# Performance work log

Hardware: AMD Instinct MI355X
Metric: run time of the kernel (lower is better)

The kernel has to match this reference:

```python
import jax, jax.numpy as jnp
import numpy as np

EMBED_DIM = 1024
HEAD_SIZE = 128


def setup_inputs() -> dict:
    key = jax.random.key(0)
    k1, k2, k3, k4 = jax.random.split(key, 4)
    B, T, C = 8, 2048, EMBED_DIM
    x = jax.random.normal(k1, (B, T, C), dtype=jnp.float32)
    # torch Linear(in, out, bias=False): weight shape [out, in]
    s = 1.0 / np.sqrt(C)
    Wk = jax.random.uniform(k2, (HEAD_SIZE, C), jnp.float32, -s, s)
    Wq = jax.random.uniform(k3, (HEAD_SIZE, C), jnp.float32, -s, s)
    Wv = jax.random.uniform(k4, (HEAD_SIZE, C), jnp.float32, -s, s)
    return {"x": x, "Wk": Wk, "Wq": Wq, "Wv": Wv}


def reference(x, Wk, Wq, Wv):
    B, T, C = x.shape
    k = jnp.einsum('btc,hc->bth', x, Wk)  # [B,T,H]
    q = jnp.einsum('btc,hc->bth', x, Wq)
    v = jnp.einsum('btc,hc->bth', x, Wv)
    # NOTE: original scales by C**-0.5 with C = embedding dim (not head size)
    w = jnp.einsum('bth,bsh->bts', q, k) * (C ** -0.5)  # [B,T,T]
    causal = jnp.tril(jnp.ones((T, T), dtype=bool))
    w = jnp.where(causal, w, -jnp.inf)
    w = jax.nn.softmax(w, axis=-1)
    return jnp.einsum('bts,bsh->bth', w, v)
```

## Files before the change

### kernel.cpp

```cpp
#include <hip/hip_runtime.h>
#include <stdint.h>

#define BATCH 8
#define SEQ   2048
#define EMB   1024
#define HD    128

typedef __attribute__((ext_vector_type(8))) short  s8v;
typedef __attribute__((ext_vector_type(4))) float  f4v;

__device__ __forceinline__ ushort cvt_bf16(float f) {
    union { float f; uint32_t u; } v; v.f = f;
    uint32_t r = v.u + 0x7FFFu + ((v.u >> 16) & 1u);
    return (ushort)(r >> 16);
}

__device__ __forceinline__ uint32_t pack_bf16(float lo, float hi) {
    return ((uint32_t)cvt_bf16(hi) << 16) | (uint32_t)cvt_bf16(lo);
}

__device__ __forceinline__ f4v mfma16(s8v a, s8v b, f4v c) {
    return __builtin_amdgcn_mfma_f32_16x16x32_bf16(a, b, c, 0, 0, 0);
}

__device__ __forceinline__ uint32_t bperm(int idx, uint32_t v) {
    return (uint32_t)__builtin_amdgcn_ds_bpermute(idx, (int)v);
}

__device__ __forceinline__ void gl_lds16(const void* g, void* l) {
    __builtin_amdgcn_global_load_lds(
        (const __attribute__((address_space(1))) void*)g,
        (__attribute__((address_space(3))) void*)l, 16, 0, 0);
}

__global__ __launch_bounds__(256) void wcvt_kernel(
    const float* __restrict__ Wk, const float* __restrict__ Wq,
    const float* __restrict__ Wv, ushort* __restrict__ Wb)
{
    const int row = blockIdx.x;
    const float* __restrict__ src =
        (row < 128) ? Wk + (size_t)row * EMB :
        (row < 256) ? Wq + (size_t)(row - 128) * EMB :
                      Wv + (size_t)(row - 256) * EMB;
    const int c = threadIdx.x << 2;
    float4 f = *(const float4*)(src + c);
    ushort4 h;
    h.x = cvt_bf16(f.x); h.y = cvt_bf16(f.y);
    h.z = cvt_bf16(f.z); h.w = cvt_bf16(f.w);
    *(ushort4*)(Wb + (size_t)row * EMB + c) = h;
}

__global__ __launch_bounds__(256) void qkv_kernel(
    const float* __restrict__ x,
    const ushort* __restrict__ Wb,
    ushort* __restrict__ Kg,
    ushort* __restrict__ Qg,
    ushort* __restrict__ VTg)
{
    const int m0 = blockIdx.x * 32;
    __shared__ ushort Al[32][68];
    __shared__ ushort Bl[384 * 64];

    const int tid  = threadIdx.x;
    const int lane = tid & 63;
    const int wave = tid >> 6;
    const int lr = lane & 15, lg = lane >> 4;
    const int xsw = (lr & 7) << 4;

    f4v acc[2][6] = {};

    const char* gW[12];
    #pragma unroll
    for (int c = 0; c < 12; ++c) {
        int cc   = wave * 12 + c;
        int row  = cc * 8 + (lane >> 3);
        int colb = ((lane & 7) << 4) ^ ((row & 7) << 4);
        gW[c] = (const char*)Wb + (size_t)row * (EMB * 2) + colb;
    }
    const int ar = tid >> 3, ac = (tid & 7) << 3;
    const float* xp = x + (size_t)(m0 + ar) * EMB + ac;

    for (int k0 = 0; k0 < EMB; k0 += 64) {
        #pragma unroll
        for (int c = 0; c < 12; ++c) {
            gl_lds16(gW[c], (char*)Bl + ((wave * 12 + c) << 10));
            gW[c] += 128;
        }
        float4 f0 = *(const float4*)(xp);
        float4 f1 = *(const float4*)(xp + 4);
        xp += 64;
        ushort4 h0, h1;
        h0.x = cvt_bf16(f0.x); h0.y = cvt_bf16(f0.y);
        h0.z = cvt_bf16(f0.z); h0.w = cvt_bf16(f0.w);
        h1.x = cvt_bf16(f1.x); h1.y = cvt_bf16(f1.y);
        h1.z = cvt_bf16(f1.z); h1.w = cvt_bf16(f1.w);
        *(ushort4*)&Al[ar][ac]     = h0;
        *(ushort4*)&Al[ar][ac + 4] = h1;
        __syncthreads();

        #pragma unroll
        for (int kk = 0; kk < 2; ++kk) {
            s8v af[2], bf[6];
            #pragma unroll
            for (int i = 0; i < 2; ++i)
                af[i] = *(const s8v*)&Al[16 * i + lr][32 * kk + 8 * lg];
            #pragma unroll
            for (int j = 0; j < 6; ++j) {
                int row = 96 * wave + 16 * j + lr;
                bf[j] = *(const s8v*)((const char*)Bl + (row << 7)
                                      + ((kk * 64 + lg * 16) ^ xsw));
            }
            #pragma unroll
            for (int i = 0; i < 2; ++i)
                #pragma unroll
                for (int j = 0; j < 6; ++j)
                    acc[i][j] = mfma16(af[i], bf[j], acc[i][j]);
        }
        __syncthreads();
    }

    const int b  = m0 >> 11;
    const int tb = m0 & 2047;
    #pragma unroll
    for (int j = 0; j < 6; ++j) {
        const int n   = 96 * wave + 16 * j + lr;
        const int sel = n >> 7;
        const int h   = n & 127;
        if (sel < 2) {
            ushort* __restrict__ outp = sel ? Qg : Kg;
            #pragma unroll
            for (int i = 0; i < 2; ++i)
                #pragma unroll
                for (int reg = 0; reg < 4; ++reg) {
                    int m = m0 + 16 * i + 4 * lg + reg;
                    outp[(size_t)m * HD + h] = cvt_bf16(acc[i][j][reg]);
                }
        } else {
            #pragma unroll
            for (int i = 0; i < 2; ++i) {
                int t = tb + 16 * i + 4 * lg;
                ushort4 hv;
                hv.x = cvt_bf16(acc[i][j][0]);
                hv.y = cvt_bf16(acc[i][j][1]);
                hv.z = cvt_bf16(acc[i][j][2]);
                hv.w = cvt_bf16(acc[i][j][3]);
                *(ushort4*)(VTg + ((size_t)b * HD + h) * SEQ + t) = hv;
            }
        }
    }
}

__global__ __launch_bounds__(256) void attn_kernel(
    const ushort* __restrict__ Qg,
    const ushort* __restrict__ Kg,
    const ushort* __restrict__ VTg,
    ushort* __restrict__ o_part,
    float2* __restrict__ ml_part,
    int cts, int NCH)
{
    int s = blockIdx.x, g = 0;
    while (s >= ((g + 1) << cts)) { s -= (g + 1) << cts; ++g; }
    int q2 = 0;
    while (s >= g + 1) { s -= g + 1; ++q2; }
    const int jq = (g << cts) + q2;
    const int ch = s;
    const int b  = blockIdx.y;
    const int t0 = ch << cts;
    const int t1 = min(t0 + (1 << cts), jq + 1);

    const int tid  = threadIdx.x;
    const int lane = tid & 63;
    const int wave = tid >> 6;
    const int lr = lane & 15, lg = lane >> 4;
    const int xsw = (lr & 7) << 4;

    __shared__ ushort kl[2][64 * 128];
    __shared__ ushort vl[2][128 * 64];

    const ushort* __restrict__ Qb = Qg  + (size_t)b * SEQ * HD;
    const ushort* __restrict__ Kb = Kg  + (size_t)b * SEQ * HD;
    const ushort* __restrict__ Vb = VTg + (size_t)b * HD * SEQ;

    const char* gK[4];
    const char* gV[4];
    #pragma unroll
    for (int c = 0; c < 4; ++c) {
        int cc = wave * 4 + c;
        {   int row  = cc * 4 + (lane >> 4);
            int colb = ((lane & 15) << 4) ^ ((row & 7) << 4);
            gK[c] = (const char*)Kb + (size_t)(t0 * 64 + row) * 256 + colb; }
        {   int row  = cc * 8 + (lane >> 3);
            int colb = ((lane & 7) << 4) ^ ((row & 7) << 4);
            gV[c] = (const char*)Vb + (size_t)row * (SEQ * 2)
                    + (size_t)t0 * 128 + colb; }
    }

    const int qw    = jq * 64 + wave * 16;
    const int q_abs = qw + lr;

    s8v qf[4];
    #pragma unroll
    for (int f = 0; f < 4; ++f)
        qf[f] = *(const s8v*)(Qb + (size_t)(qw + lr) * HD + 32 * f + 8 * lg);

    f4v o[8] = {};
    float m_r = -1e30f, l_r = 0.0f;

    #pragma unroll
    for (int c = 0; c < 4; ++c) {
        gl_lds16(gK[c], (char*)(&kl[0][0]) + ((wave * 4 + c) << 10));
        gl_lds16(gV[c], (char*)(&vl[0][0]) + ((wave * 4 + c) << 10));
        gK[c] += 64 * 256;
        gV[c] += 128;
    }
    __syncthreads();

    const int i0 = ((2 * (lg & 1)) * 16 + lr) << 2;
    const int i1 = ((2 * (lg & 1) + 1) * 16 + lr) << 2;
    const bool hi = (lg >= 2);

    int cur = 0;
    for (int st = t0; st < t1; ++st) {
        if (st + 1 < t1) {
            char* kb = (char*)(&kl[cur ^ 1][0]);
            char* vb = (char*)(&vl[cur ^ 1][0]);
            #pragma unroll
            for (int c = 0; c < 4; ++c) {
                gl_lds16(gK[c], kb + ((wave * 4 + c) << 10));
                gl_lds16(gV[c], vb + ((wave * 4 + c) << 10));
                gK[c] += 64 * 256;
                gV[c] += 128;
            }
        }
        const int s0 = st * 64;
        const char* klb = (const char*)(&kl[cur][0]);
        const char* vlb = (const char*)(&vl[cur][0]);

        f4v sc[4] = {};
        #pragma unroll
        for (int sf = 0; sf < 4; ++sf)
            #pragma unroll
            for (int kf = 0; kf < 4; ++kf) {
                s8v kfr = *(const s8v*)(klb + ((sf * 16 + lr) << 8)
                                        + ((kf * 64 + lg * 16) ^ xsw));
                sc[sf] = mfma16(kfr, qf[kf], sc[sf]);
            }

        float p[4][4];
        const bool diag = (st == jq);
        #pragma unroll
        for (int sf = 0; sf < 4; ++sf)
            #pragma unroll
            for (int reg = 0; reg < 4; ++reg) {
                float v = sc[sf][reg] * 0.03125f;
                if (diag && (s0 + sf * 16 + 4 * lg + reg) > q_abs) v = -1e30f;
                p[sf][reg] = v;
            }

        float pm = p[0][0];
        #pragma unroll
        for (int sf = 0; sf < 4; ++sf)
            #pragma unroll
            for (int reg = 0; reg < 4; ++reg) pm = fmaxf(pm, p[sf][reg]);
        pm = fmaxf(pm, __shfl_xor(pm, 16));
        pm = fmaxf(pm, __shfl_xor(pm, 32));
        const float mnew = fmaxf(m_r, pm);
        const float fac  = __expf(m_r - mnew);
        m_r = mnew;

        float ls = 0.0f;
        #pragma unroll
        for (int sf = 0; sf < 4; ++sf)
            #pragma unroll
            for (int reg = 0; reg < 4; ++reg) {
                p[sf][reg] = __expf(p[sf][reg] - mnew);
                ls += p[sf][reg];
            }
        ls += __shfl_xor(ls, 16);
        ls += __shfl_xor(ls, 32);
        l_r = l_r * fac + ls;
        #pragma unroll
        for (int hf = 0; hf < 8; ++hf) o[hf] *= fac;

        uint32_t pk[4][2];
        #pragma unroll
        for (int sf = 0; sf < 4; ++sf) {
            pk[sf][0] = pack_bf16(p[sf][0], p[sf][1]);
            pk[sf][1] = pack_bf16(p[sf][2], p[sf][3]);
        }

        #pragma unroll
        for (int s2 = 0; s2 < 2; ++s2) {
            uint32_t a0 = bperm(i0, pk[2 * s2][0]);
            uint32_t a1 = bperm(i0, pk[2 * s2][1]);
            uint32_t a2 = bperm(i1, pk[2 * s2][0]);
            uint32_t a3 = bperm(i1, pk[2 * s2][1]);
            uint32_t b0 = bperm(i0, pk[2 * s2 + 1][0]);
            uint32_t b1 = bperm(i0, pk[2 * s2 + 1][1]);
            uint32_t b2 = bperm(i1, pk[2 * s2 + 1][0]);
            uint32_t b3 = bperm(i1, pk[2 * s2 + 1][1]);
            union { int4 i; s8v h; } pb;
            pb.i.x = (int)(hi ? b0 : a0);
            pb.i.y = (int)(hi ? b1 : a1);
            pb.i.z = (int)(hi ? b2 : a2);
            pb.i.w = (int)(hi ? b3 : a3);
            #pragma unroll
            for (int hf = 0; hf < 8; ++hf) {
                s8v vf = *(const s8v*)(vlb + ((hf * 16 + lr) << 7)
                                       + ((s2 * 64 + lg * 16) ^ xsw));
                o[hf] = mfma16(vf, pb.h, o[hf]);
            }
        }

        __syncthreads();
        cur ^= 1;
    }

    const size_t pbase = ((size_t)(b * 32 + jq) * NCH + ch) * 64;
    const int q = wave * 16 + lr;
    if (lg == 0) {
        float2 v; v.x = m_r; v.y = l_r;
        ml_part[pbase + q] = v;
    }
    #pragma unroll
    for (int hf = 0; hf < 8; ++hf) {
        ushort4 hv;
        hv.x = cvt_bf16(o[hf][0]);
        hv.y = cvt_bf16(o[hf][1]);
        hv.z = cvt_bf16(o[hf][2]);
        hv.w = cvt_bf16(o[hf][3]);
        *(ushort4*)(o_part + (pbase + q) * HD + hf * 16 + 4 * lg) = hv;
    }
}

__global__ __launch_bounds__(256) void combine_kernel(
    const ushort* __restrict__ o_part,
    const float2* __restrict__ ml_part,
    float* __restrict__ out, int cts, int NCH)
{
    const int tid = threadIdx.x;
    const int R   = blockIdx.x * 16 + (tid >> 4);
    const int c16 = tid & 15;
    const int b  = R >> 11;
    const int rq = R & 2047;
    const int jq = rq >> 6;
    const int r  = rq & 63;
    const int nch = (jq >> cts) + 1;

    const size_t mlbase = ((size_t)(b * 32 + jq) * NCH) * 64 + r;

    float M = -1e30f;
    for (int c = 0; c < nch; ++c)
        M = fmaxf(M, ml_part[mlbase + (size_t)c * 64].x);
    float L = 0.0f;
    for (int c = 0; c < nch; ++c) {
        float2 v = ml_part[mlbase + (size_t)c * 64];
        L += v.y * __expf(v.x - M);
    }
    const float invL = 1.0f / L;

    float acc[8];
    #pragma unroll
    for (int k = 0; k < 8; ++k) acc[k] = 0.0f;

    for (int c = 0; c < nch; ++c) {
        float2 v = ml_part[mlbase + (size_t)c * 64];
        float sc = __expf(v.x - M) * invL;
        s8v pv = *(const s8v*)(o_part + (mlbase + (size_t)c * 64) * HD + c16 * 8);
        #pragma unroll
        for (int j = 0; j < 8; ++j) {
            union { uint32_t u; float f; } cv;
            cv.u = ((uint32_t)(ushort)pv[j]) << 16;
            acc[j] += cv.f * sc;
        }
    }

    float* po = out + (size_t)R * HD + c16 * 8;
    *(float4*)(po)     = make_float4(acc[0], acc[1], acc[2], acc[3]);
    *(float4*)(po + 4) = make_float4(acc[4], acc[5], acc[6], acc[7]);
}

extern "C" void kernel_launch(void* const* d_in, const int* in_sizes, int n_in,
                              void* d_out, int out_size, void* d_ws, size_t ws_size,
                              hipStream_t stream) {
    const float* x  = (const float*)d_in[0];
    const float* Wk = (const float*)d_in[1];
    const float* Wq = (const float*)d_in[2];
    const float* Wv = (const float*)d_in[3];

    const size_t qkv_elems = (size_t)BATCH * SEQ * HD;
    const size_t wb_elems  = (size_t)384 * EMB;
    ushort* Kg  = (ushort*)d_ws;
    ushort* Qg  = Kg + qkv_elems;
    ushort* VTg = Qg + qkv_elems;
    float*  outp = (float*)d_out;

    int cts = 2, NCH = 8;
    {
        size_t rows = (size_t)BATCH * 32 * NCH * 64;
        size_t need = 3 * qkv_elems * sizeof(ushort)
                    + rows * (HD * sizeof(ushort) + sizeof(float2))
                    + wb_elems * sizeof(ushort);
        if (ws_size < need) { cts = 3; NCH = 4; }
    }
    size_t part_rows = (size_t)BATCH * 32 * NCH * 64;
    ushort* o_part  = VTg + qkv_elems;
    float2* ml_part = (float2*)(o_part + part_rows * HD);
    ushort* Wb      = (ushort*)(ml_part + part_rows);

    const int G = 32 >> cts;
    const int slots = (1 << cts) * G * (G + 1) / 2;

    wcvt_kernel<<<384, 256, 0, stream>>>(Wk, Wq, Wv, Wb);
    qkv_kernel<<<512, 256, 0, stream>>>(x, Wb, Kg, Qg, VTg);
    dim3 g2(slots, BATCH);
    attn_kernel<<<g2, 256, 0, stream>>>(Qg, Kg, VTg, o_part, ml_part, cts, NCH);
    combine_kernel<<<1024, 256, 0, stream>>>(o_part, ml_part, outp, cts, NCH);
}
```

Baseline: 81.97 us.

## Load QKV GEMM operands directly from global into registers, dropping LDS staging

The QKV projection kernel no longer stages x and the bf16 weights through shared memory with barriers. Each lane now loads its MFMA fragments straight from global memory, converting x with packed bf16 intrinsics, and relies on the cache for reuse across waves. This removes the LDS traffic and the __syncthreads stalls. The cost is uncoalesced, strided global loads, with every wave re-reading the same x rows from cache.

```diff
diff --git a/kernel.cpp b/kernel.cpp
--- a/kernel.cpp
+++ b/kernel.cpp
@@ -1,4 +1,5 @@
 #include <hip/hip_runtime.h>
+#include <hip/hip_bf16.h>
 #include <stdint.h>
 
 #define BATCH 8
@@ -31,6 +32,15 @@
     __builtin_amdgcn_global_load_lds(
         (const __attribute__((address_space(1))) void*)g,
         (__attribute__((address_space(3))) void*)l, 16, 0, 0);
+}
+
+__device__ __forceinline__ s8v cvt8(float4 a, float4 b) {
+    union { s8v h; __hip_bfloat162 p[4]; } u;
+    u.p[0] = __float22bfloat162_rn(make_float2(a.x, a.y));
+    u.p[1] = __float22bfloat162_rn(make_float2(a.z, a.w));
+    u.p[2] = __float22bfloat162_rn(make_float2(b.x, b.y));
+    u.p[3] = __float22bfloat162_rn(make_float2(b.z, b.w));
+    return u.h;
 }
 
 __global__ __launch_bounds__(256) void wcvt_kernel(
@@ -58,65 +68,35 @@
     ushort* __restrict__ VTg)
 {
     const int m0 = blockIdx.x * 32;
-    __shared__ ushort Al[32][68];
-    __shared__ ushort Bl[384 * 64];
-
     const int tid  = threadIdx.x;
     const int lane = tid & 63;
     const int wave = tid >> 6;
     const int lr = lane & 15, lg = lane >> 4;
-    const int xsw = (lr & 7) << 4;
 
     f4v acc[2][6] = {};
 
-    const char* gW[12];
-    #pragma unroll
-    for (int c = 0; c < 12; ++c) {
-        int cc   = wave * 12 + c;
-        int row  = cc * 8 + (lane >> 3);
-        int colb = ((lane & 7) << 4) ^ ((row & 7) << 4);
-        gW[c] = (const char*)Wb + (size_t)row * (EMB * 2) + colb;
-    }
-    const int ar = tid >> 3, ac = (tid & 7) << 3;
-    const float* xp = x + (size_t)(m0 + ar) * EMB + ac;
-
-    for (int k0 = 0; k0 < EMB; k0 += 64) {
-        #pragma unroll
-        for (int c = 0; c < 12; ++c) {
-            gl_lds16(gW[c], (char*)Bl + ((wave * 12 + c) << 10));
-            gW[c] += 128;
-        }
-        float4 f0 = *(const float4*)(xp);
-        float4 f1 = *(const float4*)(xp + 4);
-        xp += 64;
-        ushort4 h0, h1;
-        h0.x = cvt_bf16(f0.x); h0.y = cvt_bf16(f0.y);
-        h0.z = cvt_bf16(f0.z); h0.w = cvt_bf16(f0.w);
-        h1.x = cvt_bf16(f1.x); h1.y = cvt_bf16(f1.y);
-        h1.z = cvt_bf16(f1.z); h1.w = cvt_bf16(f1.w);
-        *(ushort4*)&Al[ar][ac]     = h0;
-        *(ushort4*)&Al[ar][ac + 4] = h1;
-        __syncthreads();
-
-        #pragma unroll
-        for (int kk = 0; kk < 2; ++kk) {
-            s8v af[2], bf[6];
-            #pragma unroll
-            for (int i = 0; i < 2; ++i)
-                af[i] = *(const s8v*)&Al[16 * i + lr][32 * kk + 8 * lg];
-            #pragma unroll
-            for (int j = 0; j < 6; ++j) {
-                int row = 96 * wave + 16 * j + lr;
-                bf[j] = *(const s8v*)((const char*)Bl + (row << 7)
-                                      + ((kk * 64 + lg * 16) ^ xsw));
-            }
-            #pragma unroll
-            for (int i = 0; i < 2; ++i)
-                #pragma unroll
-                for (int j = 0; j < 6; ++j)
-                    acc[i][j] = mfma16(af[i], bf[j], acc[i][j]);
-        }
-        __syncthreads();
+    const float* xp0 = x + (size_t)(m0 + lr) * EMB + 8 * lg;
+    const float* xp1 = xp0 + (size_t)16 * EMB;
+    const ushort* wp0 = Wb + (size_t)(96 * wave + lr) * EMB + 8 * lg;
+
+    #pragma unroll 4
+    for (int ks = 0; ks < 32; ++ks) {
+        const int kc = ks * 32;
+        float4 a0 = *(const float4*)(xp0 + kc);
+        float4 a1 = *(const float4*)(xp0 + kc + 4);
+        float4 b0 = *(const float4*)(xp1 + kc);
+        float4 b1 = *(const float4*)(xp1 + kc + 4);
+        s8v af0 = cvt8(a0, a1);
+        s8v af1 = cvt8(b0, b1);
+        s8v bf[6];
+        #pragma unroll
+        for (int j = 0; j < 6; ++j)
+            bf[j] = *(const s8v*)(wp0 + (size_t)j * 16 * EMB + kc);
+        #pragma unroll
+        for (int j = 0; j < 6; ++j) {
+            acc[0][j] = mfma16(af0, bf[j], acc[0][j]);
+            acc[1][j] = mfma16(af1, bf[j], acc[1][j]);
+        }
     }
 
     const int b  = m0 >> 11;
```

New measurement: 127.3 us. 55.3% more time.

## Retile QKV projection into 128x128 per-weight output tiles

Applied to the files above, without the earlier changes.

The QKV GEMM now gives each block a 128-row by 128-column tile of a single projection (K, Q or V), with a 4x4 MFMA tile per wave, instead of 32 rows across all 384 output columns. This raises MFMA work per loaded element and cuts the total weight re-reads. In exchange x is read three times, and the async global-to-LDS weight loads and XOR swizzle are replaced by plain synchronous loads into padded shared memory. The grid shrinks to 384 blocks.

```diff
diff --git a/kernel.cpp b/kernel.cpp
--- a/kernel.cpp
+++ b/kernel.cpp
@@ -1,4 +1,5 @@
 #include <hip/hip_runtime.h>
+#include <hip/hip_bf16.h>
 #include <stdint.h>
 
 #define BATCH 8
@@ -57,96 +58,91 @@
     ushort* __restrict__ Qg,
     ushort* __restrict__ VTg)
 {
-    const int m0 = blockIdx.x * 32;
-    __shared__ ushort Al[32][68];
-    __shared__ ushort Bl[384 * 64];
+    const int bid  = blockIdx.x;
+    const int rest = bid >> 3;
+    const int wsel = rest % 3;
+    const int mt   = ((rest / 3) << 3) | (bid & 7);
+    const int m0 = mt * 128;
+    const ushort* __restrict__ Wp = Wb + (size_t)wsel * 128 * EMB;
+
+    __shared__ ushort Al[128][72];
+    __shared__ ushort Bl[128][72];
 
     const int tid  = threadIdx.x;
     const int lane = tid & 63;
     const int wave = tid >> 6;
+    const int wm = wave >> 1, wn = wave & 1;
     const int lr = lane & 15, lg = lane >> 4;
-    const int xsw = (lr & 7) << 4;
-
-    f4v acc[2][6] = {};
-
-    const char* gW[12];
-    #pragma unroll
-    for (int c = 0; c < 12; ++c) {
-        int cc   = wave * 12 + c;
-        int row  = cc * 8 + (lane >> 3);
-        int colb = ((lane & 7) << 4) ^ ((row & 7) << 4);
-        gW[c] = (const char*)Wb + (size_t)row * (EMB * 2) + colb;
-    }
-    const int ar = tid >> 3, ac = (tid & 7) << 3;
-    const float* xp = x + (size_t)(m0 + ar) * EMB + ac;
+
+    f4v acc[4][4] = {};
 
     for (int k0 = 0; k0 < EMB; k0 += 64) {
         #pragma unroll
-        for (int c = 0; c < 12; ++c) {
-            gl_lds16(gW[c], (char*)Bl + ((wave * 12 + c) << 10));
-            gW[c] += 128;
-        }
-        float4 f0 = *(const float4*)(xp);
-        float4 f1 = *(const float4*)(xp + 4);
-        xp += 64;
-        ushort4 h0, h1;
-        h0.x = cvt_bf16(f0.x); h0.y = cvt_bf16(f0.y);
-        h0.z = cvt_bf16(f0.z); h0.w = cvt_bf16(f0.w);
-        h1.x = cvt_bf16(f1.x); h1.y = cvt_bf16(f1.y);
-        h1.z = cvt_bf16(f1.z); h1.w = cvt_bf16(f1.w);
-        *(ushort4*)&Al[ar][ac]     = h0;
-        *(ushort4*)&Al[ar][ac + 4] = h1;
+        for (int it = 0; it < 8; ++it) {
+            int chunk = tid + 256 * it;
+            int r  = chunk >> 4;
+            int c4 = (chunk & 15) << 2;
+            float4 fa = *(const float4*)(x + (size_t)(m0 + r) * EMB + k0 + c4);
+            ushort4 ha;
+            ha.x = cvt_bf16(fa.x); ha.y = cvt_bf16(fa.y);
+            ha.z = cvt_bf16(fa.z); ha.w = cvt_bf16(fa.w);
+            *(ushort4*)&Al[r][c4] = ha;
+        }
+        #pragma unroll
+        for (int it = 0; it < 4; ++it) {
+            int chunk = tid + 256 * it;
+            int r  = chunk >> 3;
+            int c8 = (chunk & 7) << 3;
+            *(int4*)&Bl[r][c8] = *(const int4*)(Wp + (size_t)r * EMB + k0 + c8);
+        }
         __syncthreads();
-
         #pragma unroll
         for (int kk = 0; kk < 2; ++kk) {
-            s8v af[2], bf[6];
-            #pragma unroll
-            for (int i = 0; i < 2; ++i)
-                af[i] = *(const s8v*)&Al[16 * i + lr][32 * kk + 8 * lg];
-            #pragma unroll
-            for (int j = 0; j < 6; ++j) {
-                int row = 96 * wave + 16 * j + lr;
-                bf[j] = *(const s8v*)((const char*)Bl + (row << 7)
-                                      + ((kk * 64 + lg * 16) ^ xsw));
-            }
-            #pragma unroll
-            for (int i = 0; i < 2; ++i)
+            s8v af[4], bf[4];
+            #pragma unroll
+            for (int i = 0; i < 4; ++i)
+                af[i] = *(const s8v*)&Al[64 * wm + 16 * i + lr][32 * kk + 8 * lg];
+            #pragma unroll
+            for (int j = 0; j < 4; ++j)
+                bf[j] = *(const s8v*)&Bl[64 * wn + 16 * j + lr][32 * kk + 8 * lg];
+            #pragma unroll
+            for (int i = 0; i < 4; ++i)
                 #pragma unroll
-                for (int j = 0; j < 6; ++j)
+                for (int j = 0; j < 4; ++j)
                     acc[i][j] = mfma16(af[i], bf[j], acc[i][j]);
         }
         __syncthreads();
     }
 
-    const int b  = m0 >> 11;
-    const int tb = m0 & 2047;
-    #pragma unroll
-    for (int j = 0; j < 6; ++j) {
-        const int n   = 96 * wave + 16 * j + lr;
-        const int sel = n >> 7;
-        const int h   = n & 127;
-        if (sel < 2) {
-            ushort* __restrict__ outp = sel ? Qg : Kg;
-            #pragma unroll
-            for (int i = 0; i < 2; ++i)
+    if (wsel < 2) {
+        ushort* __restrict__ outp = wsel ? Qg : Kg;
+        #pragma unroll
+        for (int i = 0; i < 4; ++i)
+            #pragma unroll
+            for (int j = 0; j < 4; ++j) {
+                int h = 64 * wn + 16 * j + lr;
                 #pragma unroll
                 for (int reg = 0; reg < 4; ++reg) {
-                    int m = m0 + 16 * i + 4 * lg + reg;
+                    int m = m0 + 64 * wm + 16 * i + 4 * lg + reg;
                     outp[(size_t)m * HD + h] = cvt_bf16(acc[i][j][reg]);
                 }
-        } else {
-            #pragma unroll
-            for (int i = 0; i < 2; ++i) {
-                int t = tb + 16 * i + 4 * lg;
+            }
+    } else {
+        int bidx = m0 >> 11;
+        int tb   = m0 & 2047;
+        #pragma unroll
+        for (int i = 0; i < 4; ++i)
+            #pragma unroll
+            for (int j = 0; j < 4; ++j) {
+                int h = 64 * wn + 16 * j + lr;
+                int t = tb + 64 * wm + 16 * i + 4 * lg;
                 ushort4 hv;
                 hv.x = cvt_bf16(acc[i][j][0]);
                 hv.y = cvt_bf16(acc[i][j][1]);
                 hv.z = cvt_bf16(acc[i][j][2]);
                 hv.w = cvt_bf16(acc[i][j][3]);
-                *(ushort4*)(VTg + ((size_t)b * HD + h) * SEQ + t) = hv;
-            }
-        }
+                *(ushort4*)(VTg + ((size_t)bidx * HD + h) * SEQ + t) = hv;
+            }
     }
 }
 
@@ -412,7 +408,7 @@
     const int slots = (1 << cts) * G * (G + 1) / 2;
 
     wcvt_kernel<<<384, 256, 0, stream>>>(Wk, Wq, Wv, Wb);
-    qkv_kernel<<<512, 256, 0, stream>>>(x, Wb, Kg, Qg, VTg);
+    qkv_kernel<<<384, 256, 0, stream>>>(x, Wb, Kg, Qg, VTg);
     dim3 g2(slots, BATCH);
     attn_kernel<<<g2, 256, 0, stream>>>(Qg, Kg, VTg, o_part, ml_part, cts, NCH);
     combine_kernel<<<1024, 256, 0, stream>>>(o_part, ml_part, outp, cts, NCH);
```

Result: slower. 84.37 us (+2.9%).
